# Kernel tuning notes

Hardware: AMD Instinct MI355X
Metric: run time of the kernel (lower is better)

Reference implementation:

```python
import jax, jax.numpy as jnp
import numpy as np

FREQ = 24       # freq_size
SEG = 21        # segment_width (attention sequence length)
NSTEPS = 512
NUNITS = 512
HEADS = 2
DH = FREQ // HEADS   # 12 per-head depth
MAXD = 4             # max relative distance -> table size 2*MAXD+1 = 9
EPS = 1e-3           # keras LayerNormalization default epsilon


def _posenc(length, d):
    # sinusoidal positional encoding [length, d]
    pos = np.arange(length)[:, None].astype(np.float64)
    i = np.arange(d)[None, :]
    angle = pos / np.power(10000.0, 2 * (i // 2) / d)
    pe = np.zeros((length, d), np.float32)
    pe[:, 0::2] = np.sin(angle[:, 0::2])
    pe[:, 1::2] = np.cos(angle[:, 1::2])
    return jnp.asarray(pe)


def _ln(x, g, b):
    m = jnp.mean(x, axis=-1, keepdims=True)
    v = jnp.mean((x - m) ** 2, axis=-1, keepdims=True)
    return g * (x - m) * jax.lax.rsqrt(v + EPS) + b


def setup_inputs() -> dict:
    key = jax.random.key(0)
    ks = jax.random.split(key, 16)
    B = 64
    s = 0.05
    inp = jax.random.normal(ks[0], (B, NSTEPS, FREQ * SEG), jnp.float32)
    d = {
        'inp': inp,
        # attention q/k/v dense (activation=relu)
        'wq': jax.random.normal(ks[1], (FREQ, FREQ), jnp.float32) * s,
        'bq': jnp.zeros((FREQ,), jnp.float32),
        'wk': jax.random.normal(ks[2], (FREQ, FREQ), jnp.float32) * s,
        'bk': jnp.zeros((FREQ,), jnp.float32),
        'wv': jax.random.normal(ks[3], (FREQ, FREQ), jnp.float32) * s,
        'bv': jnp.zeros((FREQ,), jnp.float32),
        # Shaw-style relative position embeddings (shared across heads)
        'rel_k': jax.random.normal(ks[4], (2 * MAXD + 1, DH), jnp.float32) * s,
        'rel_v': jax.random.normal(ks[5], (2 * MAXD + 1, DH), jnp.float32) * s,
        'ln_attn_g': jnp.ones((FREQ,), jnp.float32),
        'ln_attn_b': jnp.zeros((FREQ,), jnp.float32),
        # feed-forward (pointwise conv1d == dense): 24 -> 96 -> 24
        'w1': jax.random.normal(ks[6], (FREQ, FREQ * 4), jnp.float32) * s,
        'b1': jnp.zeros((FREQ * 4,), jnp.float32),
        'w2': jax.random.normal(ks[7], (FREQ * 4, FREQ), jnp.float32) * s,
        'b2': jnp.zeros((FREQ,), jnp.float32),
        'ln_ff_g': jnp.ones((FREQ,), jnp.float32),
        'ln_ff_b': jnp.zeros((FREQ,), jnp.float32),
        # final dense 504 -> 512 (relu) + layernorm
        'wd': jax.random.normal(ks[8], (FREQ * SEG, NUNITS), jnp.float32) * s,
        'bd': jnp.zeros((NUNITS,), jnp.float32),
        'ln_out_g': jnp.ones((NUNITS,), jnp.float32),
        'ln_out_b': jnp.zeros((NUNITS,), jnp.float32),
    }
    return d


def reference(inp, wq, bq, wk, bk, wv, bv, rel_k, rel_v, ln_attn_g, ln_attn_b,
              w1, b1, w2, b2, ln_ff_g, ln_ff_b, wd, bd, ln_out_g, ln_out_b):
    # [B, T, 504] -> [B*T, 24, 21] -> [B*T, 21, 24]
    x = inp.reshape(-1, FREQ, SEG).transpose(0, 2, 1)
    x = x + _posenc(SEG, FREQ) * 0.01 + 0.01

    N = x.shape[0]
    q = jax.nn.relu(x @ wq + bq)
    k = jax.nn.relu(x @ wk + bk)
    v = jax.nn.relu(x @ wv + bv)
    # split heads: [N, H, L, DH]
    qh = q.reshape(N, SEG, HEADS, DH).transpose(0, 2, 1, 3)
    kh = k.reshape(N, SEG, HEADS, DH).transpose(0, 2, 1, 3)
    vh = v.reshape(N, SEG, HEADS, DH).transpose(0, 2, 1, 3)

    # relative position indices, clipped to [-MAXD, MAXD]
    r = jnp.arange(SEG)
    idx = jnp.clip(r[None, :] - r[:, None], -MAXD, MAXD) + MAXD  # [L, L]
    rk = rel_k[idx]  # [L, L, DH]
    rv = rel_v[idx]  # [L, L, DH]

    logits = (jnp.einsum('bhqd,bhkd->bhqk', qh, kh)
              + jnp.einsum('bhqd,qkd->bhqk', qh, rk)) / jnp.sqrt(jnp.float32(DH))
    w = jax.nn.softmax(logits, axis=-1)
    o = (jnp.einsum('bhqk,bhkd->bhqd', w, vh)
         + jnp.einsum('bhqk,qkd->bhqd', w, rv))
    o = o.transpose(0, 2, 1, 3).reshape(N, SEG, FREQ)
    attn = _ln(o + x, ln_attn_g, ln_attn_b)

    # feed-forward with residual + layernorm
    ff = jax.nn.relu(attn @ w1 + b1) @ w2 + b2
    ff = _ln(ff + attn, ln_ff_g, ln_ff_b)

    # [N, 21, 24] -> [N, 24, 21] -> [B, T, 504]
    out = ff.transpose(0, 2, 1).reshape(-1, NSTEPS, FREQ * SEG)
    out = jax.nn.relu(out @ wd + bd)
    return _ln(out, ln_out_g, ln_out_b)
```

## Files before the change

### kernel.cpp

```cpp
#include <hip/hip_runtime.h>
#include <math.h>

#define O_WQ   0
#define O_WK   576
#define O_WV   1152
#define O_RELK 1728
#define O_RELV 1836
#define O_W1   1944
#define O_W2   4248
#define O_BQ   6552
#define O_BK   6576
#define O_BV   6600
#define O_B1   6624
#define O_B2   6720
#define O_GA   6744
#define O_BA   6768
#define O_GF   6792
#define O_BF   6816
#define O_PE   6840
#define O_KV   7344
#define SM_TOT (O_KV + 12*504)

#define REP21(M) M(0) M(1) M(2) M(3) M(4) M(5) M(6) M(7) M(8) M(9) M(10) \
                 M(11) M(12) M(13) M(14) M(15) M(16) M(17) M(18) M(19) M(20)
#define REP24(M) REP21(M) M(21) M(22) M(23)

#define LD6(bp,A,B,C,D,E,F) \
  const float* Lb_ = (bp); \
  float4 A=*(const float4*)(Lb_+0),  B=*(const float4*)(Lb_+4),  C=*(const float4*)(Lb_+8), \
         D=*(const float4*)(Lb_+12), E=*(const float4*)(Lb_+16), F=*(const float4*)(Lb_+20);

#define FMA24(P,xs,A,B,C,D,E,F) \
  P##0 =fmaf(xs,A.x,P##0 ); P##1 =fmaf(xs,A.y,P##1 ); P##2 =fmaf(xs,A.z,P##2 ); P##3 =fmaf(xs,A.w,P##3 ); \
  P##4 =fmaf(xs,B.x,P##4 ); P##5 =fmaf(xs,B.y,P##5 ); P##6 =fmaf(xs,B.z,P##6 ); P##7 =fmaf(xs,B.w,P##7 ); \
  P##8 =fmaf(xs,C.x,P##8 ); P##9 =fmaf(xs,C.y,P##9 ); P##10=fmaf(xs,C.z,P##10); P##11=fmaf(xs,C.w,P##11); \
  P##12=fmaf(xs,D.x,P##12); P##13=fmaf(xs,D.y,P##13); P##14=fmaf(xs,D.z,P##14); P##15=fmaf(xs,D.w,P##15); \
  P##16=fmaf(xs,E.x,P##16); P##17=fmaf(xs,E.y,P##17); P##18=fmaf(xs,E.z,P##18); P##19=fmaf(xs,E.w,P##19); \
  P##20=fmaf(xs,F.x,P##20); P##21=fmaf(xs,F.y,P##21); P##22=fmaf(xs,F.z,P##22); P##23=fmaf(xs,F.w,P##23);

#define WJ(j,W,P) { const float xj_ = x##j; LD6(&sm[(W)+(j)*24], wA,wB,wC,wD,wE,wF) \
                    FMA24(P,xj_,wA,wB,wC,wD,wE,wF) }
#define REPW24(W,P) WJ(0,W,P) WJ(1,W,P) WJ(2,W,P) WJ(3,W,P) WJ(4,W,P) WJ(5,W,P) \
  WJ(6,W,P) WJ(7,W,P) WJ(8,W,P) WJ(9,W,P) WJ(10,W,P) WJ(11,W,P) WJ(12,W,P) WJ(13,W,P) \
  WJ(14,W,P) WJ(15,W,P) WJ(16,W,P) WJ(17,W,P) WJ(18,W,P) WJ(19,W,P) WJ(20,W,P) \
  WJ(21,W,P) WJ(22,W,P) WJ(23,W,P)

__global__ void posenc_kernel(float* __restrict__ pe) {
    int i = threadIdx.x;
    if (i < 504) {
        int f = i / 21, s = i % 21;
        double e = (double)(2 * (f / 2)) / 24.0;
        double ang = (double)s / pow(10000.0, e);
        float v = (f & 1) ? cosf((float)ang) : sinf((float)ang);
        pe[i] = 0.01f * v + 0.01f;
    }
}

__global__ __launch_bounds__(256, 3) void token_kernel(
    const float* __restrict__ inp,
    const float* __restrict__ wq, const float* __restrict__ bq,
    const float* __restrict__ wk, const float* __restrict__ bk,
    const float* __restrict__ wv, const float* __restrict__ bv,
    const float* __restrict__ relk, const float* __restrict__ relv,
    const float* __restrict__ ga, const float* __restrict__ ba,
    const float* __restrict__ w1, const float* __restrict__ b1,
    const float* __restrict__ w2, const float* __restrict__ b2,
    const float* __restrict__ gf, const float* __restrict__ bf,
    const float* __restrict__ pe, float* __restrict__ ffout, int ntok)
{
    __shared__ __align__(16) float sm[SM_TOT];
    const int tid  = threadIdx.x;
    const int lane = tid & 63;
    const int wv_  = tid >> 6;

    {
        const size_t lim4  = (size_t)ntok * 126;
        const size_t base4 = ((size_t)blockIdx.x * 12 + wv_ * 3) * 126;
        const float4* in4 = (const float4*)inp;
        float4* t4 = (float4*)&sm[O_KV + wv_ * 1512];
        #pragma unroll
        for (int c = 0; c < 6; ++c) {
            int idx = lane + c * 64;
            if (idx < 378) {
                float4 v4 = make_float4(0.f, 0.f, 0.f, 0.f);
                if (base4 + idx < lim4) v4 = in4[base4 + idx];
                t4[idx] = v4;
            }
        }
    }

    for (int i = tid; i < 576; i += 256) { sm[O_WQ+i]=wq[i]; sm[O_WK+i]=wk[i]; sm[O_WV+i]=wv[i]; }
    for (int i = tid; i < 2304; i += 256) { sm[O_W1+i]=w1[i]; sm[O_W2+i]=w2[i]; }
    if (tid < 108) { sm[O_RELK+tid]=relk[tid]; sm[O_RELV+tid]=relv[tid]; }
    if (tid < 24) { sm[O_BQ+tid]=bq[tid]; sm[O_BK+tid]=bk[tid]; sm[O_BV+tid]=bv[tid];
                    sm[O_B2+tid]=b2[tid]; sm[O_GA+tid]=ga[tid]; sm[O_BA+tid]=ba[tid];
                    sm[O_GF+tid]=gf[tid]; sm[O_BF+tid]=bf[tid]; }
    if (tid >= 128 && tid < 224) sm[O_B1+tid-128] = b1[tid-128];
    for (int i = tid; i < 504; i += 256) sm[O_PE+i] = pe[i];
    __syncthreads();

    int t = lane / 21;
    int s = lane - t * 21;
    if (lane == 63) { t = 2; s = 20; }
    float* tile  = &sm[O_KV + (wv_*3 + t) * 504];
    float* myrow = tile + s * 24;

#define DX(i) float x##i = tile[(i)*21 + s] + sm[O_PE + (i)*21 + s];
    REP24(DX)

    {
#define DKK(i) float kk##i = sm[O_BK+(i)];
        REP24(DKK)
        REPW24(O_WK, kk)
        *(float4*)(myrow+ 0) = make_float4(fmaxf(kk0 ,0.f),fmaxf(kk1 ,0.f),fmaxf(kk2 ,0.f),fmaxf(kk3 ,0.f));
        *(float4*)(myrow+ 4) = make_float4(fmaxf(kk4 ,0.f),fmaxf(kk5 ,0.f),fmaxf(kk6 ,0.f),fmaxf(kk7 ,0.f));
        *(float4*)(myrow+ 8) = make_float4(fmaxf(kk8 ,0.f),fmaxf(kk9 ,0.f),fmaxf(kk10,0.f),fmaxf(kk11,0.f));
        *(float4*)(myrow+12) = make_float4(fmaxf(kk12,0.f),fmaxf(kk13,0.f),fmaxf(kk14,0.f),fmaxf(kk15,0.f));
        *(float4*)(myrow+16) = make_float4(fmaxf(kk16,0.f),fmaxf(kk17,0.f),fmaxf(kk18,0.f),fmaxf(kk19,0.f));
        *(float4*)(myrow+20) = make_float4(fmaxf(kk20,0.f),fmaxf(kk21,0.f),fmaxf(kk22,0.f),fmaxf(kk23,0.f));
    }

#define DQQ(i) float q##i = sm[O_BQ+(i)];
    REP24(DQQ)
    REPW24(O_WQ, q)
#define RQ(i) q##i = fmaxf(q##i, 0.f);
    REP24(RQ)
    asm volatile("s_waitcnt lgkmcnt(0)" ::: "memory");

#define DP_(i) float p0_##i, p1_##i;
    REP21(DP_)
#define LGT(ks) { \
    int dd=(ks)-s; dd=dd<-4?-4:(dd>4?4:dd); dd+=4; \
    const float* kr_ = tile + (ks)*24; \
    const float* rr_ = &sm[O_RELK + dd*12]; \
    LD6(kr_, kA,kB,kC,kD,kE,kF) \
    float4 rA=*(const float4*)(rr_+0), rB=*(const float4*)(rr_+4), rC=*(const float4*)(rr_+8); \
    float a0_=0.f, a1_=0.f; \
    a0_=fmaf(q0 ,kA.x+rA.x,a0_); a0_=fmaf(q1 ,kA.y+rA.y,a0_); a0_=fmaf(q2 ,kA.z+rA.z,a0_); a0_=fmaf(q3 ,kA.w+rA.w,a0_); \
    a0_=fmaf(q4 ,kB.x+rB.x,a0_); a0_=fmaf(q5 ,kB.y+rB.y,a0_); a0_=fmaf(q6 ,kB.z+rB.z,a0_); a0_=fmaf(q7 ,kB.w+rB.w,a0_); \
    a0_=fmaf(q8 ,kC.x+rC.x,a0_); a0_=fmaf(q9 ,kC.y+rC.y,a0_); a0_=fmaf(q10,kC.z+rC.z,a0_); a0_=fmaf(q11,kC.w+rC.w,a0_); \
    a1_=fmaf(q12,kD.x+rA.x,a1_); a1_=fmaf(q13,kD.y+rA.y,a1_); a1_=fmaf(q14,kD.z+rA.z,a1_); a1_=fmaf(q15,kD.w+rA.w,a1_); \
    a1_=fmaf(q16,kE.x+rB.x,a1_); a1_=fmaf(q17,kE.y+rB.y,a1_); a1_=fmaf(q18,kE.z+rB.z,a1_); a1_=fmaf(q19,kE.w+rB.w,a1_); \
    a1_=fmaf(q20,kF.x+rC.x,a1_); a1_=fmaf(q21,kF.y+rC.y,a1_); a1_=fmaf(q22,kF.z+rC.z,a1_); a1_=fmaf(q23,kF.w+rC.w,a1_); \
    p0_##ks = a0_*0.28867513459481287f; p1_##ks = a1_*0.28867513459481287f; }
    REP21(LGT)

    {
        float m0 = p0_0, m1 = p1_0;
#define MX(i) m0 = fmaxf(m0, p0_##i); m1 = fmaxf(m1, p1_##i);
        REP21(MX)
        float sum0 = 0.f, sum1 = 0.f;
#define EX(i) p0_##i = __expf(p0_##i - m0); sum0 += p0_##i; \
              p1_##i = __expf(p1_##i - m1); sum1 += p1_##i;
        REP21(EX)
        float is0 = 1.f/sum0, is1 = 1.f/sum1;
#define NM(i) p0_##i *= is0; p1_##i *= is1;
        REP21(NM)
    }

    asm volatile("s_waitcnt lgkmcnt(0)" ::: "memory");
    {
#define DVV(i) float vv##i = sm[O_BV+(i)];
        REP24(DVV)
        REPW24(O_WV, vv)
        *(float4*)(myrow+ 0) = make_float4(fmaxf(vv0 ,0.f),fmaxf(vv1 ,0.f),fmaxf(vv2 ,0.f),fmaxf(vv3 ,0.f));
        *(float4*)(myrow+ 4) = make_float4(fmaxf(vv4 ,0.f),fmaxf(vv5 ,0.f),fmaxf(vv6 ,0.f),fmaxf(vv7 ,0.f));
        *(float4*)(myrow+ 8) = make_float4(fmaxf(vv8 ,0.f),fmaxf(vv9 ,0.f),fmaxf(vv10,0.f),fmaxf(vv11,0.f));
        *(float4*)(myrow+12) = make_float4(fmaxf(vv12,0.f),fmaxf(vv13,0.f),fmaxf(vv14,0.f),fmaxf(vv15,0.f));
        *(float4*)(myrow+16) = make_float4(fmaxf(vv16,0.f),fmaxf(vv17,0.f),fmaxf(vv18,0.f),fmaxf(vv19,0.f));
        *(float4*)(myrow+20) = make_float4(fmaxf(vv20,0.f),fmaxf(vv21,0.f),fmaxf(vv22,0.f),fmaxf(vv23,0.f));
    }
    asm volatile("s_waitcnt lgkmcnt(0)" ::: "memory");

#define DO_(i) float o##i = 0.f;
    REP24(DO_)
#define OT(ks) { \
    int dd=(ks)-s; dd=dd<-4?-4:(dd>4?4:dd); dd+=4; \
    const float* vr_ = tile + (ks)*24; \
    const float* rr_ = &sm[O_RELV + dd*12]; \
    LD6(vr_, vA,vB,vC,vD,vE,vF) \
    float4 rA=*(const float4*)(rr_+0), rB=*(const float4*)(rr_+4), rC=*(const float4*)(rr_+8); \
    const float w0_ = p0_##ks, w1_ = p1_##ks; \
    o0 =fmaf(w0_,vA.x+rA.x,o0 ); o1 =fmaf(w0_,vA.y+rA.y,o1 ); o2 =fmaf(w0_,vA.z+rA.z,o2 ); o3 =fmaf(w0_,vA.w+rA.w,o3 ); \
    o4 =fmaf(w0_,vB.x+rB.x,o4 ); o5 =fmaf(w0_,vB.y+rB.y,o5 ); o6 =fmaf(w0_,vB.z+rB.z,o6 ); o7 =fmaf(w0_,vB.w+rB.w,o7 ); \
    o8 =fmaf(w0_,vC.x+rC.x,o8 ); o9 =fmaf(w0_,vC.y+rC.y,o9 ); o10=fmaf(w0_,vC.z+rC.z,o10); o11=fmaf(w0_,vC.w+rC.w,o11); \
    o12=fmaf(w1_,vD.x+rA.x,o12); o13=fmaf(w1_,vD.y+rA.y,o13); o14=fmaf(w1_,vD.z+rA.z,o14); o15=fmaf(w1_,vD.w+rA.w,o15); \
    o16=fmaf(w1_,vE.x+rB.x,o16); o17=fmaf(w1_,vE.y+rB.y,o17); o18=fmaf(w1_,vE.z+rB.z,o18); o19=fmaf(w1_,vE.w+rB.w,o19); \
    o20=fmaf(w1_,vF.x+rC.x,o20); o21=fmaf(w1_,vF.y+rC.y,o21); o22=fmaf(w1_,vF.z+rC.z,o22); o23=fmaf(w1_,vF.w+rC.w,o23); }
    REP21(OT)

#define ATD(i) float at##i = o##i + x##i;
    REP24(ATD)
    {
        float sA = 0.f, sB = 0.f;
#define ASUM(i) sA += at##i; sB = fmaf(at##i, at##i, sB);
        REP24(ASUM)
        float mn = sA * (1.f/24.f);
        float rstd = rsqrtf(sB*(1.f/24.f) - mn*mn + 1e-3f);
#define ALN(i) at##i = fmaf(sm[O_GA+(i)], (at##i - mn)*rstd, sm[O_BA+(i)]);
        REP24(ALN)
    }

#define DFF(i) float ff##i = sm[O_B2+(i)];
    REP24(DFF)
    for (int cc = 0; cc < 96; cc += 24) {
#define DH2(i) float h##i = sm[O_B1 + cc + (i)];
        REP24(DH2)
#define HJ(j) { const float aj_ = at##j; LD6(&sm[O_W1+(j)*96+cc], wA,wB,wC,wD,wE,wF) \
                FMA24(h,aj_,wA,wB,wC,wD,wE,wF) }
        REP24(HJ)
#define RH(i) h##i = fmaxf(h##i, 0.f);
        REP24(RH)
#define FL(l) { const float hl_ = h##l; LD6(&sm[O_W2+(cc+(l))*24], wA,wB,wC,wD,wE,wF) \
                FMA24(ff,hl_,wA,wB,wC,wD,wE,wF) }
        REP24(FL)
    }

    {
#define FR(i) ff##i += at##i;
        REP24(FR)
        float sC = 0.f, sD = 0.f;
#define FSUM(i) sC += ff##i; sD = fmaf(ff##i, ff##i, sD);
        REP24(FSUM)
        float mn2 = sC * (1.f/24.f);
        float rstd2 = rsqrtf(sD*(1.f/24.f) - mn2*mn2 + 1e-3f);
#define FLN(i) ff##i = fmaf(sm[O_GF+(i)], (ff##i - mn2)*rstd2, sm[O_BF+(i)]);
        REP24(FLN)
    }

#define STF(i) tile[(i)*21 + s] = ff##i;
    REP24(STF)
    asm volatile("s_waitcnt lgkmcnt(0)" ::: "memory");
    {
        const size_t lim4  = (size_t)ntok * 126;
        const size_t base4 = ((size_t)blockIdx.x * 12 + wv_ * 3) * 126;
        float4* out4 = (float4*)ffout;
        const float4* t4 = (const float4*)&sm[O_KV + wv_ * 1512];
        #pragma unroll
        for (int c = 0; c < 6; ++c) {
            int idx = lane + c * 64;
            if (idx < 378 && base4 + idx < lim4)
                out4[base4 + idx] = t4[idx];
        }
    }
}

#define DB_LDA 68
__global__ __launch_bounds__(256, 2) void dense_kernel(
    const float* __restrict__ A, const float* __restrict__ wd,
    const float* __restrict__ bd, float* __restrict__ out)
{
    __shared__ __align__(16) float At[24*DB_LDA];
    __shared__ __align__(16) float Bs[24*512];
    const int tid  = threadIdx.x;
    const int w    = tid >> 6;
    const int lane = tid & 63;
    const int lr   = lane >> 3;
    const int lc   = lane & 7;
    const int row0 = blockIdx.x * 64;
    const int colb = w*128 + lc*4;

    float acc[8][16];
    #pragma unroll
    for (int r = 0; r < 8; ++r)
        #pragma unroll
        for (int j = 0; j < 16; ++j) acc[r][j] = 0.f;

    for (int k0 = 0; k0 < 504; k0 += 24) {
        __syncthreads();
        #pragma unroll
        for (int i = 0; i < 6; ++i) {
            int ii = tid + i*256;
            int r = ii / 24, kk = ii - r*24;
            At[kk*DB_LDA + r] = A[(size_t)(row0 + r)*504 + k0 + kk];
        }
        const float4* Bg = (const float4*)(wd + k0*512);
        float4* Bs4 = (float4*)Bs;
        #pragma unroll
        for (int i = 0; i < 12; ++i) Bs4[tid + i*256] = Bg[tid + i*256];
        __syncthreads();

        #pragma unroll 4
        for (int kk = 0; kk < 24; ++kk) {
            float4 a0 = *(const float4*)&At[kk*DB_LDA + lr*8];
            float4 a1 = *(const float4*)&At[kk*DB_LDA + lr*8 + 4];
            float av[8] = {a0.x,a0.y,a0.z,a0.w,a1.x,a1.y,a1.z,a1.w};
            float bv[16];
            #pragma unroll
            for (int cb = 0; cb < 4; ++cb) {
                float4 b4 = *(const float4*)&Bs[kk*512 + colb + cb*32];
                bv[cb*4+0]=b4.x; bv[cb*4+1]=b4.y; bv[cb*4+2]=b4.z; bv[cb*4+3]=b4.w;
            }
            #pragma unroll
            for (int r = 0; r < 8; ++r)
                #pragma unroll
                for (int j = 0; j < 16; ++j)
                    acc[r][j] = fmaf(av[r], bv[j], acc[r][j]);
        }
    }

    float4 bias[4];
    #pragma unroll
    for (int cb = 0; cb < 4; ++cb) bias[cb] = *(const float4*)&bd[colb + cb*32];
    #pragma unroll
    for (int r = 0; r < 8; ++r) {
        float* orow = out + (size_t)(row0 + lr*8 + r)*512;
        #pragma unroll
        for (int cb = 0; cb < 4; ++cb) {
            float4 o4;
            o4.x = fmaxf(acc[r][cb*4+0] + bias[cb].x, 0.f);
            o4.y = fmaxf(acc[r][cb*4+1] + bias[cb].y, 0.f);
            o4.z = fmaxf(acc[r][cb*4+2] + bias[cb].z, 0.f);
            o4.w = fmaxf(acc[r][cb*4+3] + bias[cb].w, 0.f);
            *(float4*)&orow[colb + cb*32] = o4;
        }
    }
}

__global__ __launch_bounds__(256, 4) void ln512_kernel(
    float* __restrict__ out, const float* __restrict__ g, const float* __restrict__ b)
{
    const int lane = threadIdx.x & 63;
    const size_t row = (size_t)blockIdx.x * 4 + (threadIdx.x >> 6);
    float4* p = (float4*)(out + row*512) + lane*2;
    float4 v0 = p[0], v1 = p[1];
    float s1 = v0.x+v0.y+v0.z+v0.w + v1.x+v1.y+v1.z+v1.w;
    float s2 = 0.f;
    s2 = fmaf(v0.x,v0.x,s2); s2 = fmaf(v0.y,v0.y,s2); s2 = fmaf(v0.z,v0.z,s2); s2 = fmaf(v0.w,v0.w,s2);
    s2 = fmaf(v1.x,v1.x,s2); s2 = fmaf(v1.y,v1.y,s2); s2 = fmaf(v1.z,v1.z,s2); s2 = fmaf(v1.w,v1.w,s2);
    #pragma unroll
    for (int off = 32; off > 0; off >>= 1) {
        s1 += __shfl_xor(s1, off);
        s2 += __shfl_xor(s2, off);
    }
    float m  = s1 * (1.f/512.f);
    float rs = rsqrtf(s2 * (1.f/512.f) - m*m + 1e-3f);
    const float4* g4 = (const float4*)g + lane*2;
    const float4* b4 = (const float4*)b + lane*2;
    float4 ga0 = g4[0], ga1 = g4[1], bb0 = b4[0], bb1 = b4[1];
    v0.x = fmaf(ga0.x, (v0.x-m)*rs, bb0.x);
    v0.y = fmaf(ga0.y, (v0.y-m)*rs, bb0.y);
    v0.z = fmaf(ga0.z, (v0.z-m)*rs, bb0.z);
    v0.w = fmaf(ga0.w, (v0.w-m)*rs, bb0.w);
    v1.x = fmaf(ga1.x, (v1.x-m)*rs, bb1.x);
    v1.y = fmaf(ga1.y, (v1.y-m)*rs, bb1.y);
    v1.z = fmaf(ga1.z, (v1.z-m)*rs, bb1.z);
    v1.w = fmaf(ga1.w, (v1.w-m)*rs, bb1.w);
    p[0] = v0; p[1] = v1;
}

extern "C" void kernel_launch(void* const* d_in, const int* in_sizes, int n_in,
                              void* d_out, int out_size, void* d_ws, size_t ws_size,
                              hipStream_t stream)
{
    const float* inp  = (const float*)d_in[0];
    const float* wq   = (const float*)d_in[1];
    const float* bq   = (const float*)d_in[2];
    const float* wk   = (const float*)d_in[3];
    const float* bk   = (const float*)d_in[4];
    const float* wv   = (const float*)d_in[5];
    const float* bv   = (const float*)d_in[6];
    const float* relk = (const float*)d_in[7];
    const float* relv = (const float*)d_in[8];
    const float* ga   = (const float*)d_in[9];
    const float* ba   = (const float*)d_in[10];
    const float* w1   = (const float*)d_in[11];
    const float* b1   = (const float*)d_in[12];
    const float* w2   = (const float*)d_in[13];
    const float* b2   = (const float*)d_in[14];
    const float* gf   = (const float*)d_in[15];
    const float* bf   = (const float*)d_in[16];
    const float* wd   = (const float*)d_in[17];
    const float* bd   = (const float*)d_in[18];
    const float* go_  = (const float*)d_in[19];
    const float* bo_  = (const float*)d_in[20];

    float* ws = (float*)d_ws;
    float* pe = ws;
    float* ff = ws + 512;
    const int N = in_sizes[0] / 504;

    hipLaunchKernelGGL(posenc_kernel, dim3(1), dim3(512), 0, stream, pe);
    hipLaunchKernelGGL(token_kernel, dim3((N + 11) / 12), dim3(256), 0, stream,
                       inp, wq, bq, wk, bk, wv, bv, relk, relv, ga, ba,
                       w1, b1, w2, b2, gf, bf, pe, ff, N);
    hipLaunchKernelGGL(dense_kernel, dim3(N/64), dim3(256), 0, stream,
                       ff, wd, bd, (float*)d_out);
    hipLaunchKernelGGL(ln512_kernel, dim3(N/4), dim3(256), 0, stream,
                       (float*)d_out, go_, bo_);
}
```

Baseline: 808.4 us.

## Cut register pressure in token kernel and split dense GEMM over column tiles

The token kernel stops keeping the 24 input values in registers. It re-reads them from a separate shared-memory input buffer, splits the per-head logit and output loops into two passes, and narrows the FFN hidden chunk to 12. This is meant to lower register pressure, though launch bounds drop to 2 blocks per SM and shared memory per block grows. The dense kernel is split into two 256-column tiles on a 2D grid with an 8x8 accumulator per thread and 4-block occupancy, doubling the grid for better latency hiding at the cost of loading A twice.

```diff
diff --git a/kernel.cpp b/kernel.cpp
--- a/kernel.cpp
+++ b/kernel.cpp
@@ -18,27 +18,33 @@
 #define O_GF   6792
 #define O_BF   6816
 #define O_PE   6840
-#define O_KV   7344
-#define SM_TOT (O_KV + 12*504)
-
-#define REP21(M) M(0) M(1) M(2) M(3) M(4) M(5) M(6) M(7) M(8) M(9) M(10) \
-                 M(11) M(12) M(13) M(14) M(15) M(16) M(17) M(18) M(19) M(20)
+#define O_IN   7344
+#define O_KV   13392
+#define SM_TOT 19440
+
+#define REP8(M)  M(0) M(1) M(2) M(3) M(4) M(5) M(6) M(7)
+#define REP12(M) REP8(M) M(8) M(9) M(10) M(11)
+#define REP21(M) REP12(M) M(12) M(13) M(14) M(15) M(16) M(17) M(18) M(19) M(20)
 #define REP24(M) REP21(M) M(21) M(22) M(23)
 
-#define LD6(bp,A,B,C,D,E,F) \
-  const float* Lb_ = (bp); \
-  float4 A=*(const float4*)(Lb_+0),  B=*(const float4*)(Lb_+4),  C=*(const float4*)(Lb_+8), \
-         D=*(const float4*)(Lb_+12), E=*(const float4*)(Lb_+16), F=*(const float4*)(Lb_+20);
-
-#define FMA24(P,xs,A,B,C,D,E,F) \
+#define LD3(bp,A,B,C) \
+  float4 A=*(const float4*)((bp)+0), B=*(const float4*)((bp)+4), C=*(const float4*)((bp)+8);
+#define LD6(bp,A,B,C,D,E,F) LD3(bp,A,B,C) \
+  float4 D=*(const float4*)((bp)+12), E=*(const float4*)((bp)+16), F=*(const float4*)((bp)+20);
+
+#define FMA12L(P,xs,A,B,C) \
   P##0 =fmaf(xs,A.x,P##0 ); P##1 =fmaf(xs,A.y,P##1 ); P##2 =fmaf(xs,A.z,P##2 ); P##3 =fmaf(xs,A.w,P##3 ); \
   P##4 =fmaf(xs,B.x,P##4 ); P##5 =fmaf(xs,B.y,P##5 ); P##6 =fmaf(xs,B.z,P##6 ); P##7 =fmaf(xs,B.w,P##7 ); \
-  P##8 =fmaf(xs,C.x,P##8 ); P##9 =fmaf(xs,C.y,P##9 ); P##10=fmaf(xs,C.z,P##10); P##11=fmaf(xs,C.w,P##11); \
-  P##12=fmaf(xs,D.x,P##12); P##13=fmaf(xs,D.y,P##13); P##14=fmaf(xs,D.z,P##14); P##15=fmaf(xs,D.w,P##15); \
-  P##16=fmaf(xs,E.x,P##16); P##17=fmaf(xs,E.y,P##17); P##18=fmaf(xs,E.z,P##18); P##19=fmaf(xs,E.w,P##19); \
-  P##20=fmaf(xs,F.x,P##20); P##21=fmaf(xs,F.y,P##21); P##22=fmaf(xs,F.z,P##22); P##23=fmaf(xs,F.w,P##23);
-
-#define WJ(j,W,P) { const float xj_ = x##j; LD6(&sm[(W)+(j)*24], wA,wB,wC,wD,wE,wF) \
+  P##8 =fmaf(xs,C.x,P##8 ); P##9 =fmaf(xs,C.y,P##9 ); P##10=fmaf(xs,C.z,P##10); P##11=fmaf(xs,C.w,P##11);
+#define FMA12H(P,xs,A,B,C) \
+  P##12=fmaf(xs,A.x,P##12); P##13=fmaf(xs,A.y,P##13); P##14=fmaf(xs,A.z,P##14); P##15=fmaf(xs,A.w,P##15); \
+  P##16=fmaf(xs,B.x,P##16); P##17=fmaf(xs,B.y,P##17); P##18=fmaf(xs,B.z,P##18); P##19=fmaf(xs,B.w,P##19); \
+  P##20=fmaf(xs,C.x,P##20); P##21=fmaf(xs,C.y,P##21); P##22=fmaf(xs,C.z,P##22); P##23=fmaf(xs,C.w,P##23);
+#define FMA24(P,xs,A,B,C,D,E,F) FMA12L(P,xs,A,B,C) FMA12H(P,xs,D,E,F)
+
+#define XR(j) (tin[(j)*21 + s] + sm[O_PE + (j)*21 + s])
+
+#define WJ(j,W,P) { const float xj_ = XR(j); LD6(&sm[(W)+(j)*24], wA,wB,wC,wD,wE,wF) \
                     FMA24(P,xj_,wA,wB,wC,wD,wE,wF) }
 #define REPW24(W,P) WJ(0,W,P) WJ(1,W,P) WJ(2,W,P) WJ(3,W,P) WJ(4,W,P) WJ(5,W,P) \
   WJ(6,W,P) WJ(7,W,P) WJ(8,W,P) WJ(9,W,P) WJ(10,W,P) WJ(11,W,P) WJ(12,W,P) WJ(13,W,P) \
@@ -56,7 +62,7 @@
     }
 }
 
-__global__ __launch_bounds__(256, 3) void token_kernel(
+__global__ __launch_bounds__(256, 2) void token_kernel(
     const float* __restrict__ inp,
     const float* __restrict__ wq, const float* __restrict__ bq,
     const float* __restrict__ wk, const float* __restrict__ bk,
@@ -77,7 +83,7 @@
         const size_t lim4  = (size_t)ntok * 126;
         const size_t base4 = ((size_t)blockIdx.x * 12 + wv_ * 3) * 126;
         const float4* in4 = (const float4*)inp;
-        float4* t4 = (float4*)&sm[O_KV + wv_ * 1512];
+        float4* t4 = (float4*)&sm[O_IN + wv_ * 1512];
         #pragma unroll
         for (int c = 0; c < 6; ++c) {
             int idx = lane + c * 64;
@@ -102,11 +108,9 @@
     int t = lane / 21;
     int s = lane - t * 21;
     if (lane == 63) { t = 2; s = 20; }
-    float* tile  = &sm[O_KV + (wv_*3 + t) * 504];
-    float* myrow = tile + s * 24;
-
-#define DX(i) float x##i = tile[(i)*21 + s] + sm[O_PE + (i)*21 + s];
-    REP24(DX)
+    const float* tin = &sm[O_IN + (wv_*3 + t) * 504];
+    float* kvt   = &sm[O_KV + (wv_*3 + t) * 504];
+    float* myrow = kvt + s * 24;
 
     {
 #define DKK(i) float kk##i = sm[O_BK+(i)];
@@ -127,23 +131,29 @@
     REP24(RQ)
     asm volatile("s_waitcnt lgkmcnt(0)" ::: "memory");
 
+    const float rsc = 0.28867513459481287f;
 #define DP_(i) float p0_##i, p1_##i;
     REP21(DP_)
-#define LGT(ks) { \
+#define LGT0(ks) { \
     int dd=(ks)-s; dd=dd<-4?-4:(dd>4?4:dd); dd+=4; \
-    const float* kr_ = tile + (ks)*24; \
-    const float* rr_ = &sm[O_RELK + dd*12]; \
-    LD6(kr_, kA,kB,kC,kD,kE,kF) \
-    float4 rA=*(const float4*)(rr_+0), rB=*(const float4*)(rr_+4), rC=*(const float4*)(rr_+8); \
-    float a0_=0.f, a1_=0.f; \
-    a0_=fmaf(q0 ,kA.x+rA.x,a0_); a0_=fmaf(q1 ,kA.y+rA.y,a0_); a0_=fmaf(q2 ,kA.z+rA.z,a0_); a0_=fmaf(q3 ,kA.w+rA.w,a0_); \
-    a0_=fmaf(q4 ,kB.x+rB.x,a0_); a0_=fmaf(q5 ,kB.y+rB.y,a0_); a0_=fmaf(q6 ,kB.z+rB.z,a0_); a0_=fmaf(q7 ,kB.w+rB.w,a0_); \
-    a0_=fmaf(q8 ,kC.x+rC.x,a0_); a0_=fmaf(q9 ,kC.y+rC.y,a0_); a0_=fmaf(q10,kC.z+rC.z,a0_); a0_=fmaf(q11,kC.w+rC.w,a0_); \
-    a1_=fmaf(q12,kD.x+rA.x,a1_); a1_=fmaf(q13,kD.y+rA.y,a1_); a1_=fmaf(q14,kD.z+rA.z,a1_); a1_=fmaf(q15,kD.w+rA.w,a1_); \
-    a1_=fmaf(q16,kE.x+rB.x,a1_); a1_=fmaf(q17,kE.y+rB.y,a1_); a1_=fmaf(q18,kE.z+rB.z,a1_); a1_=fmaf(q19,kE.w+rB.w,a1_); \
-    a1_=fmaf(q20,kF.x+rC.x,a1_); a1_=fmaf(q21,kF.y+rC.y,a1_); a1_=fmaf(q22,kF.z+rC.z,a1_); a1_=fmaf(q23,kF.w+rC.w,a1_); \
-    p0_##ks = a0_*0.28867513459481287f; p1_##ks = a1_*0.28867513459481287f; }
-    REP21(LGT)
+    LD3(kvt + (ks)*24, kA,kB,kC) \
+    LD3(&sm[O_RELK + dd*12], rA,rB,rC) \
+    float a_=0.f; \
+    a_=fmaf(q0 ,kA.x+rA.x,a_); a_=fmaf(q1 ,kA.y+rA.y,a_); a_=fmaf(q2 ,kA.z+rA.z,a_); a_=fmaf(q3 ,kA.w+rA.w,a_); \
+    a_=fmaf(q4 ,kB.x+rB.x,a_); a_=fmaf(q5 ,kB.y+rB.y,a_); a_=fmaf(q6 ,kB.z+rB.z,a_); a_=fmaf(q7 ,kB.w+rB.w,a_); \
+    a_=fmaf(q8 ,kC.x+rC.x,a_); a_=fmaf(q9 ,kC.y+rC.y,a_); a_=fmaf(q10,kC.z+rC.z,a_); a_=fmaf(q11,kC.w+rC.w,a_); \
+    p0_##ks = a_*rsc; }
+    REP21(LGT0)
+#define LGT1(ks) { \
+    int dd=(ks)-s; dd=dd<-4?-4:(dd>4?4:dd); dd+=4; \
+    LD3(kvt + (ks)*24 + 12, kA,kB,kC) \
+    LD3(&sm[O_RELK + dd*12], rA,rB,rC) \
+    float a_=0.f; \
+    a_=fmaf(q12,kA.x+rA.x,a_); a_=fmaf(q13,kA.y+rA.y,a_); a_=fmaf(q14,kA.z+rA.z,a_); a_=fmaf(q15,kA.w+rA.w,a_); \
+    a_=fmaf(q16,kB.x+rB.x,a_); a_=fmaf(q17,kB.y+rB.y,a_); a_=fmaf(q18,kB.z+rB.z,a_); a_=fmaf(q19,kB.w+rB.w,a_); \
+    a_=fmaf(q20,kC.x+rC.x,a_); a_=fmaf(q21,kC.y+rC.y,a_); a_=fmaf(q22,kC.z+rC.z,a_); a_=fmaf(q23,kC.w+rC.w,a_); \
+    p1_##ks = a_*rsc; }
+    REP21(LGT1)
 
     {
         float m0 = p0_0, m1 = p1_0;
@@ -174,22 +184,26 @@
 
 #define DO_(i) float o##i = 0.f;
     REP24(DO_)
-#define OT(ks) { \
+#define OT0(ks) { \
     int dd=(ks)-s; dd=dd<-4?-4:(dd>4?4:dd); dd+=4; \
-    const float* vr_ = tile + (ks)*24; \
-    const float* rr_ = &sm[O_RELV + dd*12]; \
-    LD6(vr_, vA,vB,vC,vD,vE,vF) \
-    float4 rA=*(const float4*)(rr_+0), rB=*(const float4*)(rr_+4), rC=*(const float4*)(rr_+8); \
-    const float w0_ = p0_##ks, w1_ = p1_##ks; \
-    o0 =fmaf(w0_,vA.x+rA.x,o0 ); o1 =fmaf(w0_,vA.y+rA.y,o1 ); o2 =fmaf(w0_,vA.z+rA.z,o2 ); o3 =fmaf(w0_,vA.w+rA.w,o3 ); \
-    o4 =fmaf(w0_,vB.x+rB.x,o4 ); o5 =fmaf(w0_,vB.y+rB.y,o5 ); o6 =fmaf(w0_,vB.z+rB.z,o6 ); o7 =fmaf(w0_,vB.w+rB.w,o7 ); \
-    o8 =fmaf(w0_,vC.x+rC.x,o8 ); o9 =fmaf(w0_,vC.y+rC.y,o9 ); o10=fmaf(w0_,vC.z+rC.z,o10); o11=fmaf(w0_,vC.w+rC.w,o11); \
-    o12=fmaf(w1_,vD.x+rA.x,o12); o13=fmaf(w1_,vD.y+rA.y,o13); o14=fmaf(w1_,vD.z+rA.z,o14); o15=fmaf(w1_,vD.w+rA.w,o15); \
-    o16=fmaf(w1_,vE.x+rB.x,o16); o17=fmaf(w1_,vE.y+rB.y,o17); o18=fmaf(w1_,vE.z+rB.z,o18); o19=fmaf(w1_,vE.w+rB.w,o19); \
-    o20=fmaf(w1_,vF.x+rC.x,o20); o21=fmaf(w1_,vF.y+rC.y,o21); o22=fmaf(w1_,vF.z+rC.z,o22); o23=fmaf(w1_,vF.w+rC.w,o23); }
-    REP21(OT)
-
-#define ATD(i) float at##i = o##i + x##i;
+    LD3(kvt + (ks)*24, vA,vB,vC) \
+    LD3(&sm[O_RELV + dd*12], rA,rB,rC) \
+    const float w_ = p0_##ks; \
+    o0 =fmaf(w_,vA.x+rA.x,o0 ); o1 =fmaf(w_,vA.y+rA.y,o1 ); o2 =fmaf(w_,vA.z+rA.z,o2 ); o3 =fmaf(w_,vA.w+rA.w,o3 ); \
+    o4 =fmaf(w_,vB.x+rB.x,o4 ); o5 =fmaf(w_,vB.y+rB.y,o5 ); o6 =fmaf(w_,vB.z+rB.z,o6 ); o7 =fmaf(w_,vB.w+rB.w,o7 ); \
+    o8 =fmaf(w_,vC.x+rC.x,o8 ); o9 =fmaf(w_,vC.y+rC.y,o9 ); o10=fmaf(w_,vC.z+rC.z,o10); o11=fmaf(w_,vC.w+rC.w,o11); }
+    REP21(OT0)
+#define OT1(ks) { \
+    int dd=(ks)-s; dd=dd<-4?-4:(dd>4?4:dd); dd+=4; \
+    LD3(kvt + (ks)*24 + 12, vA,vB,vC) \
+    LD3(&sm[O_RELV + dd*12], rA,rB,rC) \
+    const float w_ = p1_##ks; \
+    o12=fmaf(w_,vA.x+rA.x,o12); o13=fmaf(w_,vA.y+rA.y,o13); o14=fmaf(w_,vA.z+rA.z,o14); o15=fmaf(w_,vA.w+rA.w,o15); \
+    o16=fmaf(w_,vB.x+rB.x,o16); o17=fmaf(w_,vB.y+rB.y,o17); o18=fmaf(w_,vB.z+rB.z,o18); o19=fmaf(w_,vB.w+rB.w,o19); \
+    o20=fmaf(w_,vC.x+rC.x,o20); o21=fmaf(w_,vC.y+rC.y,o21); o22=fmaf(w_,vC.z+rC.z,o22); o23=fmaf(w_,vC.w+rC.w,o23); }
+    REP21(OT1)
+
+#define ATD(i) float at##i = o##i + XR(i);
     REP24(ATD)
     {
         float sA = 0.f, sB = 0.f;
@@ -203,17 +217,18 @@
 
 #define DFF(i) float ff##i = sm[O_B2+(i)];
     REP24(DFF)
-    for (int cc = 0; cc < 96; cc += 24) {
-#define DH2(i) float h##i = sm[O_B1 + cc + (i)];
-        REP24(DH2)
-#define HJ(j) { const float aj_ = at##j; LD6(&sm[O_W1+(j)*96+cc], wA,wB,wC,wD,wE,wF) \
-                FMA24(h,aj_,wA,wB,wC,wD,wE,wF) }
+    for (int cc = 0; cc < 96; cc += 12) {
+#define DH(i) float h##i = sm[O_B1 + cc + (i)];
+        REP12(DH)
+#define HJ(j) { const float aj_ = at##j; LD3(&sm[O_W1+(j)*96+cc], wA,wB,wC) \
+                FMA12L(h,aj_,wA,wB,wC) }
         REP24(HJ)
 #define RH(i) h##i = fmaxf(h##i, 0.f);
-        REP24(RH)
-#define FL(l) { const float hl_ = h##l; LD6(&sm[O_W2+(cc+(l))*24], wA,wB,wC,wD,wE,wF) \
-                FMA24(ff,hl_,wA,wB,wC,wD,wE,wF) }
-        REP24(FL)
+        REP12(RH)
+#define FL(l) { const float hl_ = h##l; \
+                { LD3(&sm[O_W2+(cc+(l))*24], wA,wB,wC) FMA12L(ff,hl_,wA,wB,wC) } \
+                { LD3(&sm[O_W2+(cc+(l))*24+12], wD,wE,wF) FMA12H(ff,hl_,wD,wE,wF) } }
+        REP12(FL)
     }
 
     {
@@ -228,7 +243,7 @@
         REP24(FLN)
     }
 
-#define STF(i) tile[(i)*21 + s] = ff##i;
+#define STF(i) kvt[(i)*21 + s] = ff##i;
     REP24(STF)
     asm volatile("s_waitcnt lgkmcnt(0)" ::: "memory");
     {
@@ -245,26 +260,27 @@
     }
 }
 
-#define DB_LDA 68
-__global__ __launch_bounds__(256, 2) void dense_kernel(
+#define DN_LDA 68
+__global__ __launch_bounds__(256, 4) void dense_kernel(
     const float* __restrict__ A, const float* __restrict__ wd,
     const float* __restrict__ bd, float* __restrict__ out)
 {
-    __shared__ __align__(16) float At[24*DB_LDA];
-    __shared__ __align__(16) float Bs[24*512];
+    __shared__ __align__(16) float At[24*DN_LDA];
+    __shared__ __align__(16) float Bs[24*256];
     const int tid  = threadIdx.x;
     const int w    = tid >> 6;
     const int lane = tid & 63;
     const int lr   = lane >> 3;
     const int lc   = lane & 7;
     const int row0 = blockIdx.x * 64;
-    const int colb = w*128 + lc*4;
-
-    float acc[8][16];
+    const int col0 = blockIdx.y * 256;
+    const int wcol = w*64 + lc*8;
+
+    float acc[8][8];
     #pragma unroll
     for (int r = 0; r < 8; ++r)
         #pragma unroll
-        for (int j = 0; j < 16; ++j) acc[r][j] = 0.f;
+        for (int j = 0; j < 8; ++j) acc[r][j] = 0.f;
 
     for (int k0 = 0; k0 < 504; k0 += 24) {
         __syncthreads();
@@ -272,48 +288,50 @@
         for (int i = 0; i < 6; ++i) {
             int ii = tid + i*256;
             int r = ii / 24, kk = ii - r*24;
-            At[kk*DB_LDA + r] = A[(size_t)(row0 + r)*504 + k0 + kk];
+            At[kk*DN_LDA + r] = A[(size_t)(row0 + r)*504 + k0 + kk];
         }
-        const float4* Bg = (const float4*)(wd + k0*512);
+        const float4* wd4 = (const float4*)wd;
         float4* Bs4 = (float4*)Bs;
         #pragma unroll
-        for (int i = 0; i < 12; ++i) Bs4[tid + i*256] = Bg[tid + i*256];
+        for (int c = 0; c < 6; ++c) {
+            int idx = tid + c*256;
+            int kk = idx >> 6, c4 = idx & 63;
+            Bs4[kk*64 + c4] = wd4[(size_t)(k0 + kk)*128 + (col0 >> 2) + c4];
+        }
         __syncthreads();
 
-        #pragma unroll 4
+        #pragma unroll
         for (int kk = 0; kk < 24; ++kk) {
-            float4 a0 = *(const float4*)&At[kk*DB_LDA + lr*8];
-            float4 a1 = *(const float4*)&At[kk*DB_LDA + lr*8 + 4];
+            float4 a0 = *(const float4*)&At[kk*DN_LDA + lr*8];
+            float4 a1 = *(const float4*)&At[kk*DN_LDA + lr*8 + 4];
+            float4 b0 = *(const float4*)&Bs[kk*256 + wcol];
+            float4 b1 = *(const float4*)&Bs[kk*256 + wcol + 4];
             float av[8] = {a0.x,a0.y,a0.z,a0.w,a1.x,a1.y,a1.z,a1.w};
-            float bv[16];
-            #pragma unroll
-            for (int cb = 0; cb < 4; ++cb) {
-                float4 b4 = *(const float4*)&Bs[kk*512 + colb + cb*32];
-                bv[cb*4+0]=b4.x; bv[cb*4+1]=b4.y; bv[cb*4+2]=b4.z; bv[cb*4+3]=b4.w;
-            }
+            float bv[8] = {b0.x,b0.y,b0.z,b0.w,b1.x,b1.y,b1.z,b1.w};
             #pragma unroll
             for (int r = 0; r < 8; ++r)
                 #pragma unroll
-                for (int j = 0; j < 16; ++j)
+                for (int j = 0; j < 8; ++j)
                     acc[r][j] = fmaf(av[r], bv[j], acc[r][j]);
         }
     }
 
-    float4 bias[4];
-    #pragma unroll
-    for (int cb = 0; cb < 4; ++cb) bias[cb] = *(const float4*)&bd[colb + cb*32];
+    float4 bias0 = *(const float4*)&bd[col0 + wcol];
+    float4 bias1 = *(const float4*)&bd[col0 + wcol + 4];
     #pragma unroll
     for (int r = 0; r < 8; ++r) {
-        float* orow = out + (size_t)(row0 + lr*8 + r)*512;
-        #pragma unroll
-        for (int cb = 0; cb < 4; ++cb) {
-            float4 o4;
-            o4.x = fmaxf(acc[r][cb*4+0] + bias[cb].x, 0.f);
-            o4.y = fmaxf(acc[r][cb*4+1] + bias[cb].y, 0.f);
-            o4.z = fmaxf(acc[r][cb*4+2] + bias[cb].z, 0.f);
-            o4.w = fmaxf(acc[r][cb*4+3] + bias[cb].w, 0.f);
-            *(float4*)&orow[colb + cb*32] = o4;
-        }
+        float* orow = out + (size_t)(row0 + lr*8 + r)*512 + col0;
+        float4 o4;
+        o4.x = fmaxf(acc[r][0] + bias0.x, 0.f);
+        o4.y = fmaxf(acc[r][1] + bias0.y, 0.f);
+        o4.z = fmaxf(acc[r][2] + bias0.z, 0.f);
+        o4.w = fmaxf(acc[r][3] + bias0.w, 0.f);
+        *(float4*)&orow[wcol] = o4;
+        o4.x = fmaxf(acc[r][4] + bias1.x, 0.f);
+        o4.y = fmaxf(acc[r][5] + bias1.y, 0.f);
+        o4.z = fmaxf(acc[r][6] + bias1.z, 0.f);
+        o4.w = fmaxf(acc[r][7] + bias1.w, 0.f);
+        *(float4*)&orow[wcol + 4] = o4;
     }
 }
 
@@ -384,7 +402,7 @@
     hipLaunchKernelGGL(token_kernel, dim3((N + 11) / 12), dim3(256), 0, stream,
                        inp, wq, bq, wk, bk, wv, bv, relk, relv, ga, ba,
                        w1, b1, w2, b2, gf, bf, pe, ff, N);
-    hipLaunchKernelGGL(dense_kernel, dim3(N/64), dim3(256), 0, stream,
+    hipLaunchKernelGGL(dense_kernel, dim3(N/64, 2), dim3(256), 0, stream,
                        ff, wd, bd, (float*)d_out);
     hipLaunchKernelGGL(ln512_kernel, dim3(N/4), dim3(256), 0, stream,
                        (float*)d_out, go_, bo_);
```

Measured after the change: 863.1 us. 6.8% more time.
